# Kernel optimization log

Hardware: AMD Instinct MI355X
Metric: run time of the kernel (lower is better)

The kernel has to match this reference:

```python
import jax, jax.numpy as jnp
import numpy as np

N_GRAPHS = 8
EPS_BN = 1e-5


def _gat(x, src, dst, W, a_src, a_dst, bias, heads, out_dim):
    # PyG GATConv: linear -> per-edge leaky-relu attention -> segment softmax over dst -> scatter-sum
    N = x.shape[0]
    h = (x @ W).reshape(N, heads, out_dim)                      # [N,H,C]
    al_s = (h * a_src).sum(-1)                                  # [N,H]
    al_d = (h * a_dst).sum(-1)                                  # [N,H]
    e = jax.nn.leaky_relu(al_s[src] + al_d[dst], 0.2)           # [E,H]
    e_max = jax.ops.segment_max(e, dst, num_segments=N)         # [N,H]
    e = jnp.exp(e - e_max[dst])
    denom = jax.ops.segment_sum(e, dst, num_segments=N)         # [N,H]
    alpha = e / (denom[dst] + 1e-16)                            # [E,H]
    msg = h[src] * alpha[:, :, None]                            # [E,H,C]
    out = jax.ops.segment_sum(msg, dst, num_segments=N)         # [N,H,C]
    return out.reshape(N, heads * out_dim) + bias


def _bn(h, gamma, beta):
    # BatchNorm over nodes, training-mode (batch stats, biased var)
    m = h.mean(0)
    v = jnp.mean((h - m) ** 2, axis=0)
    return (h - m) * jax.lax.rsqrt(v + EPS_BN) * gamma + beta


def setup_inputs() -> dict:
    key = jax.random.key(0)
    ks = jax.random.split(key, 24)
    N, F, H, HD, E, B, A = 50000, 64, 4, 64, 400000, N_GRAPHS, 4
    D = H * HD  # 256
    x = jax.random.normal(ks[0], (N, F), dtype=jnp.float32)
    edge_index = jax.random.randint(ks[1], (2, E), 0, N, dtype=jnp.int32)
    batch_index = jnp.sort(jax.random.randint(ks[2], (N,), 0, B, dtype=jnp.int32))
    target_node_idx = jax.random.randint(ks[3], (B,), 0, N, dtype=jnp.int32)
    s = lambda k, shp, sc: jax.random.normal(k, shp, dtype=jnp.float32) * sc
    params = {
        "W1": s(ks[4], (F, D), 0.1), "a1_src": s(ks[5], (1, H, HD), 0.1),
        "a1_dst": s(ks[6], (1, H, HD), 0.1), "b1": jnp.zeros((D,), jnp.float32),
        "W2": s(ks[7], (D, D), 0.05), "a2_src": s(ks[8], (1, 1, D), 0.1),
        "a2_dst": s(ks[9], (1, 1, D), 0.1), "b2": jnp.zeros((D,), jnp.float32),
        "g1": jnp.ones((D,), jnp.float32), "be1": jnp.zeros((D,), jnp.float32),
        "g2": jnp.ones((D,), jnp.float32), "be2": jnp.zeros((D,), jnp.float32),
        "W_sh": s(ks[10], (D, D), 0.05), "b_sh": jnp.zeros((D,), jnp.float32),
        "W_node": s(ks[11], (2 * D, 1), 0.01), "b_node": jnp.zeros((1,), jnp.float32),
        "W_type": s(ks[12], (2 * D, A), 0.01), "b_type": jnp.zeros((A,), jnp.float32),
        "W_crit": s(ks[13], (D, 1), 0.05), "b_crit": jnp.zeros((1,), jnp.float32),
    }
    return {"x": x, "edge_index": edge_index, "batch_index": batch_index,
            "target_node_idx": target_node_idx, **params}


def reference(x, edge_index, batch_index, target_node_idx,
              W1, a1_src, a1_dst, b1, W2, a2_src, a2_dst, b2,
              g1, be1, g2, be2, W_sh, b_sh, W_node, b_node,
              W_type, b_type, W_crit, b_crit):
    N = x.shape[0]
    loop = jnp.arange(N, dtype=edge_index.dtype)  # GATConv adds self-loops by default
    src = jnp.concatenate([edge_index[0], loop])
    dst = jnp.concatenate([edge_index[1], loop])

    h = jax.nn.relu(_bn(_gat(x, src, dst, W1, a1_src, a1_dst, b1, 4, 64), g1, be1))
    x_nodes = jax.nn.relu(_bn(_gat(h, src, dst, W2, a2_src, a2_dst, b2, 1, 256), g2, be2))

    # global_mean_pool
    ones = jnp.ones((N,), x.dtype)
    cnt = jax.ops.segment_sum(ones, batch_index, num_segments=N_GRAPHS)
    sums = jax.ops.segment_sum(x_nodes, batch_index, num_segments=N_GRAPHS)
    global_feat = sums / jnp.maximum(cnt, 1.0)[:, None]          # [B,256]
    shared = jax.nn.relu(global_feat @ W_sh + b_sh)              # [B,256]

    node_ctx = jnp.concatenate([x_nodes, shared[batch_index]], axis=1)   # [N,512]
    node_scores = (node_ctx @ W_node + b_node).squeeze(-1)               # [N]

    combined = jnp.concatenate([shared, x_nodes[target_node_idx]], axis=1)  # [B,512]
    type_logits = combined @ W_type + b_type                                # [B,4]
    value = shared @ W_crit + b_crit                                        # [B,1]
    return node_scores, type_logits, value
```

## Files before the change

kernel.cpp:

```cpp
#include <hip/hip_runtime.h>

typedef unsigned short u16;
typedef __attribute__((ext_vector_type(8))) short bf16x8;
typedef __attribute__((ext_vector_type(4))) float f32x4;

#define NPART 64
#define CAP 32

__device__ __forceinline__ float bf2f(u16 u) {
    return __uint_as_float(((unsigned int)u) << 16);
}
__device__ __forceinline__ u16 f2bf(float f) {
    unsigned int u = __float_as_uint(f);
    u += 0x7fffu + ((u >> 16) & 1u);
    return (u16)(u >> 16);
}
__device__ __forceinline__ bf16x8 pack8(float4 a, float4 b) {
    bf16x8 r;
    r[0] = (short)f2bf(a.x); r[1] = (short)f2bf(a.y);
    r[2] = (short)f2bf(a.z); r[3] = (short)f2bf(a.w);
    r[4] = (short)f2bf(b.x); r[5] = (short)f2bf(b.y);
    r[6] = (short)f2bf(b.z); r[7] = (short)f2bf(b.w);
    return r;
}
__device__ __forceinline__ void fma8(float* acc, float a, int4 v) {
    unsigned vx = (unsigned)v.x, vy = (unsigned)v.y, vz = (unsigned)v.z, vw = (unsigned)v.w;
    acc[0] = fmaf(a, bf2f((u16)(vx & 0xffff)), acc[0]);
    acc[1] = fmaf(a, bf2f((u16)(vx >> 16)), acc[1]);
    acc[2] = fmaf(a, bf2f((u16)(vy & 0xffff)), acc[2]);
    acc[3] = fmaf(a, bf2f((u16)(vy >> 16)), acc[3]);
    acc[4] = fmaf(a, bf2f((u16)(vz & 0xffff)), acc[4]);
    acc[5] = fmaf(a, bf2f((u16)(vz >> 16)), acc[5]);
    acc[6] = fmaf(a, bf2f((u16)(vw & 0xffff)), acc[6]);
    acc[7] = fmaf(a, bf2f((u16)(vw >> 16)), acc[7]);
}

__global__ __launch_bounds__(256) void packW_kernel(const float* __restrict__ W1,
                                                    const float* __restrict__ W2,
                                                    u16* __restrict__ out1,
                                                    u16* __restrict__ out2,
                                                    const int* __restrict__ batch,
                                                    int N, int* __restrict__ bnds) {
    const int total1 = 16 * 2 * 512;
    const int total2 = 16 * 8 * 512;
    int idx = (int)blockIdx.x * 256 + threadIdx.x;
    if (idx >= total1 + total2) {
        int i = idx - (total1 + total2);
        if (i < N) {
            int b = batch[i];
            int bp = (i == 0) ? -1 : batch[i - 1];
            for (int g2 = bp + 1; g2 <= b; g2++) bnds[g2] = i;
            if (i == N - 1)
                for (int g2 = b + 1; g2 <= 8; g2++) bnds[g2] = N;
        }
        return;
    }
    const float* W;
    u16* out;
    int KS, id;
    if (idx < total1) { W = W1; out = out1; KS = 2; id = idx; }
    else { W = W2; out = out2; KS = 8; id = idx - total1; }
    int j = id & 7;
    int lane = (id >> 3) & 63;
    int rest = id >> 9;
    int ks = rest % KS;
    int ct = rest / KS;
    int k = ks * 32 + (lane >> 4) * 8 + j;
    int n = ct * 16 + (lane & 15);
    out[id] = f2bf(W[k * 256 + n]);
}

template <int K, int H, int MODE>
__global__ __launch_bounds__(256) void gemm_mfma(const void* __restrict__ Ain,
                                                 const u16* __restrict__ Bp,
                                                 u16* __restrict__ O,
                                                 const float* __restrict__ as_,
                                                 const float* __restrict__ ad_,
                                                 float* __restrict__ als,
                                                 float* __restrict__ ald,
                                                 const float* __restrict__ bsum,
                                                 const float* __restrict__ bsq,
                                                 const float* __restrict__ g,
                                                 const float* __restrict__ be,
                                                 int Nrows,
                                                 const int* __restrict__ ei2,
                                                 int E2,
                                                 int* __restrict__ cursor,
                                                 u16* __restrict__ csr,
                                                 int scatterBlocks) {
    constexpr int KS = K / 32;
    __shared__ u16 lds[4][32 * 256];
    __shared__ float sc_s[256], sh_s[256];
    if (MODE == 0) {
        if ((int)blockIdx.x < scatterBlocks) {
            int i = blockIdx.x * 256 + threadIdx.x;
            if (i < E2) {
                int d = ei2[E2 + i];
                int p = atomicAdd(&cursor[d], 1);
                if (p < CAP) csr[(size_t)d * CAP + p] = (u16)ei2[i];
            } else if (i < E2 + Nrows) {
                int n = i - E2;
                int p = atomicAdd(&cursor[n], 1);
                if (p < CAP) csr[(size_t)n * CAP + p] = (u16)n;
            }
            return;
        }
    }
    if (MODE == 1) {
        int t = threadIdx.x;
        float mmS = 0.f, qqS = 0.f;
        for (int k2 = 0; k2 < NPART; k2++) {
            mmS += bsum[k2 * 256 + t];
            qqS += bsq[k2 * 256 + t];
        }
        float inv = 1.f / (float)Nrows;
        float mm = mmS * inv;
        float vv = fmaxf(qqS * inv - mm * mm, 0.f);
        float sc = rsqrtf(vv + 1e-5f) * g[t];
        sc_s[t] = sc;
        sh_s[t] = be[t] - mm * sc;
        __syncthreads();
    }
    int wave = threadIdx.x >> 6, lane = threadIdx.x & 63;
    int tile = ((int)blockIdx.x - (MODE == 0 ? scatterBlocks : 0)) * 4 + wave;
    int row0 = tile * 32;
    if (row0 >= Nrows) return;
    int m = lane & 15, q = lane >> 4;
    int r0c = min(row0 + m, Nrows - 1);
    int r1c = min(row0 + 16 + m, Nrows - 1);

    bf16x8 af0[KS], af1[KS];
    if (MODE == 0) {
        const float* A = (const float*)Ain;
        const float* a0 = A + (size_t)r0c * K + q * 8;
        const float* a1 = A + (size_t)r1c * K + q * 8;
#pragma unroll
        for (int ks = 0; ks < KS; ks++) {
            af0[ks] = pack8(*(const float4*)(a0 + ks * 32), *(const float4*)(a0 + ks * 32 + 4));
            af1[ks] = pack8(*(const float4*)(a1 + ks * 32), *(const float4*)(a1 + ks * 32 + 4));
        }
    } else {
        const u16* A = (const u16*)Ain;
        const u16* a0 = A + (size_t)r0c * K + q * 8;
        const u16* a1 = A + (size_t)r1c * K + q * 8;
#pragma unroll
        for (int ks = 0; ks < KS; ks++) {
            int cb = ks * 32 + q * 8;
            float4 sc0 = *(const float4*)&sc_s[cb];
            float4 sc1 = *(const float4*)&sc_s[cb + 4];
            float4 sh0 = *(const float4*)&sh_s[cb];
            float4 sh1 = *(const float4*)&sh_s[cb + 4];
            ushort4 u0 = *(const ushort4*)(a0 + ks * 32);
            ushort4 u1 = *(const ushort4*)(a0 + ks * 32 + 4);
            float4 v0 = make_float4(fmaxf(fmaf(bf2f(u0.x), sc0.x, sh0.x), 0.f),
                                    fmaxf(fmaf(bf2f(u0.y), sc0.y, sh0.y), 0.f),
                                    fmaxf(fmaf(bf2f(u0.z), sc0.z, sh0.z), 0.f),
                                    fmaxf(fmaf(bf2f(u0.w), sc0.w, sh0.w), 0.f));
            float4 v1 = make_float4(fmaxf(fmaf(bf2f(u1.x), sc1.x, sh1.x), 0.f),
                                    fmaxf(fmaf(bf2f(u1.y), sc1.y, sh1.y), 0.f),
                                    fmaxf(fmaf(bf2f(u1.z), sc1.z, sh1.z), 0.f),
                                    fmaxf(fmaf(bf2f(u1.w), sc1.w, sh1.w), 0.f));
            af0[ks] = pack8(v0, v1);
            ushort4 w0 = *(const ushort4*)(a1 + ks * 32);
            ushort4 w1 = *(const ushort4*)(a1 + ks * 32 + 4);
            float4 x0 = make_float4(fmaxf(fmaf(bf2f(w0.x), sc0.x, sh0.x), 0.f),
                                    fmaxf(fmaf(bf2f(w0.y), sc0.y, sh0.y), 0.f),
                                    fmaxf(fmaf(bf2f(w0.z), sc0.z, sh0.z), 0.f),
                                    fmaxf(fmaf(bf2f(w0.w), sc0.w, sh0.w), 0.f));
            float4 x1 = make_float4(fmaxf(fmaf(bf2f(w1.x), sc1.x, sh1.x), 0.f),
                                    fmaxf(fmaf(bf2f(w1.y), sc1.y, sh1.y), 0.f),
                                    fmaxf(fmaf(bf2f(w1.z), sc1.z, sh1.z), 0.f),
                                    fmaxf(fmaf(bf2f(w1.w), sc1.w, sh1.w), 0.f));
            af1[ks] = pack8(x0, x1);
        }
    }

    u16* myl = lds[wave];
#pragma unroll
    for (int ct2 = 0; ct2 < 8; ct2++) {
        int ct0 = ct2 * 2;
        f32x4 a00 = {0.f, 0.f, 0.f, 0.f}, a01 = {0.f, 0.f, 0.f, 0.f};
        f32x4 a10 = {0.f, 0.f, 0.f, 0.f}, a11 = {0.f, 0.f, 0.f, 0.f};
        const u16* bp0 = Bp + ((size_t)(ct0 * KS) * 64 + lane) * 8;
        const u16* bp1 = bp0 + (size_t)KS * 512;
#pragma unroll
        for (int ks = 0; ks < KS; ks++) {
            bf16x8 b0 = *(const bf16x8*)(bp0 + (size_t)ks * 512);
            bf16x8 b1 = *(const bf16x8*)(bp1 + (size_t)ks * 512);
            a00 = __builtin_amdgcn_mfma_f32_16x16x32_bf16(af0[ks], b0, a00, 0, 0, 0);
            a01 = __builtin_amdgcn_mfma_f32_16x16x32_bf16(af0[ks], b1, a01, 0, 0, 0);
            a10 = __builtin_amdgcn_mfma_f32_16x16x32_bf16(af1[ks], b0, a10, 0, 0, 0);
            a11 = __builtin_amdgcn_mfma_f32_16x16x32_bf16(af1[ks], b1, a11, 0, 0, 0);
        }
#pragma unroll
        for (int r = 0; r < 4; r++) {
            myl[(q * 4 + r) * 256 + ct0 * 16 + m] = f2bf(a00[r]);
            myl[(q * 4 + r) * 256 + ct0 * 16 + 16 + m] = f2bf(a01[r]);
            myl[(16 + q * 4 + r) * 256 + ct0 * 16 + m] = f2bf(a10[r]);
            myl[(16 + q * 4 + r) * 256 + ct0 * 16 + 16 + m] = f2bf(a11[r]);
        }
    }
    int c8 = (lane & 31) * 8;
    float4 s0 = *(const float4*)(as_ + c8);
    float4 s1 = *(const float4*)(as_ + c8 + 4);
    float4 d0 = *(const float4*)(ad_ + c8);
    float4 d1 = *(const float4*)(ad_ + c8 + 4);
#pragma unroll
    for (int p = 0; p < 16; p++) {
        int row = p * 2 + (lane >> 5);
        if (row0 + row >= Nrows) continue;
        int4 v = *(const int4*)&myl[row * 256 + c8];
        *(int4*)&O[(size_t)(row0 + row) * 256 + c8] = v;
        float f0 = bf2f((u16)(v.x & 0xffff)), f1 = bf2f((u16)((unsigned)v.x >> 16));
        float f2 = bf2f((u16)(v.y & 0xffff)), f3 = bf2f((u16)((unsigned)v.y >> 16));
        float f4 = bf2f((u16)(v.z & 0xffff)), f5 = bf2f((u16)((unsigned)v.z >> 16));
        float f6 = bf2f((u16)(v.w & 0xffff)), f7 = bf2f((u16)((unsigned)v.w >> 16));
        float ps = f0 * s0.x + f1 * s0.y + f2 * s0.z + f3 * s0.w +
                   f4 * s1.x + f5 * s1.y + f6 * s1.z + f7 * s1.w;
        float pd = f0 * d0.x + f1 * d0.y + f2 * d0.z + f3 * d0.w +
                   f4 * d1.x + f5 * d1.y + f6 * d1.z + f7 * d1.w;
        const int W = (H == 4) ? 8 : 32;
#pragma unroll
        for (int o = 1; o < W; o <<= 1) {
            ps += __shfl_xor(ps, o);
            pd += __shfl_xor(pd, o);
        }
        if (H == 4) {
            if ((lane & 7) == 0) {
                int head = (lane & 31) >> 3;
                als[(row0 + row) * 4 + head] = ps;
                ald[(row0 + row) * 4 + head] = pd;
            }
        } else {
            if ((lane & 31) == 0) {
                als[row0 + row] = ps;
                ald[row0 + row] = pd;
            }
        }
    }
}

template <int H>
__global__ __launch_bounds__(256) void gat_fused_kernel(const int* __restrict__ cnt,
                                                        const u16* __restrict__ csr,
                                                        const float* __restrict__ als,
                                                        const float* __restrict__ ald,
                                                        const u16* __restrict__ h,
                                                        u16* __restrict__ out, int N,
                                                        float* __restrict__ sum_p,
                                                        float* __restrict__ sq_p) {
    constexpr int PRE = 12;
    __shared__ float lalpha[8][32 * H];
    __shared__ int lsrc[8][32];
    __shared__ float lbuf[8][256];
    int hw = threadIdx.x >> 5;
    int lane = threadIdx.x & 31;
    int w = (blockIdx.x * 256 + threadIdx.x) >> 5;
    bool active = (w < N);
    int wc = active ? w : (N - 1);
    int deg = active ? min(cnt[wc], CAP) : 0;
    int s0 = wc * CAP;
    int s1 = s0 + deg;
    int cend = min(deg, 32);
    int npre = min(cend, PRE);
    float adl[H], e0[H], m[H], den[H];
#pragma unroll
    for (int hh = 0; hh < H; hh++) {
        adl[hh] = active ? ald[wc * H + hh] : 0.f;
        m[hh] = -1e30f;
    }
    int i0 = s0 + lane;
    bool have = active && (i0 < s1);
    int src0 = have ? (int)csr[i0] : (active ? (int)csr[s0] : 0);
    const int4* h16 = (const int4*)h;
    int4 hreg[PRE];
#pragma unroll
    for (int j = 0; j < PRE; j++) {
        int s = __shfl(src0, j, 32);
        if (j < npre) hreg[j] = h16[(size_t)s * 32 + lane];
    }
    if (have) {
        if (H == 4) {
            float4 av = ((const float4*)als)[src0];
            float tmp[4] = {av.x, av.y, av.z, av.w};
#pragma unroll
            for (int hh = 0; hh < 4; hh++) {
                float e = tmp[hh] + adl[hh];
                e = e > 0.f ? e : 0.2f * e;
                e0[hh] = e; m[hh] = e;
            }
        } else {
            float e = als[src0] + adl[0];
            e = e > 0.f ? e : 0.2f * e;
            e0[0] = e; m[0] = e;
        }
    }
    for (int i = i0 + 32; i < s1; i += 32) {
        int s = (int)csr[i];
#pragma unroll
        for (int hh = 0; hh < H; hh++) {
            float e = als[s * H + hh] + adl[hh];
            e = e > 0.f ? e : 0.2f * e;
            m[hh] = fmaxf(m[hh], e);
        }
    }
#pragma unroll
    for (int hh = 0; hh < H; hh++)
        for (int o = 16; o; o >>= 1) m[hh] = fmaxf(m[hh], __shfl_xor(m[hh], o));
#pragma unroll
    for (int hh = 0; hh < H; hh++) den[hh] = have ? __expf(e0[hh] - m[hh]) : 0.f;
    for (int i = i0 + 32; i < s1; i += 32) {
        int s = (int)csr[i];
#pragma unroll
        for (int hh = 0; hh < H; hh++) {
            float e = als[s * H + hh] + adl[hh];
            e = e > 0.f ? e : 0.2f * e;
            den[hh] += __expf(e - m[hh]);
        }
    }
#pragma unroll
    for (int hh = 0; hh < H; hh++)
        for (int o = 16; o; o >>= 1) den[hh] += __shfl_xor(den[hh], o);
    float rden[H];
#pragma unroll
    for (int hh = 0; hh < H; hh++) rden[hh] = 1.f / (den[hh] + 1e-16f);
    if (have) {
        lsrc[hw][lane] = src0;
#pragma unroll
        for (int hh = 0; hh < H; hh++)
            lalpha[hw][lane * H + hh] = __expf(e0[hh] - m[hh]) * rden[hh];
    }
    int myh = (H == 4) ? (lane >> 3) : 0;
    const float* la = lalpha[hw];
    const int* ls = lsrc[hw];
    float acc[8];
#pragma unroll
    for (int k2 = 0; k2 < 8; k2++) acc[k2] = 0.f;
#pragma unroll
    for (int j = 0; j < PRE; j++)
        if (j < npre) fma8(acc, la[j * H + myh], hreg[j]);
    int i = npre;
    for (; i + 4 <= cend; i += 4) {
        int sa = ls[i], sb = ls[i + 1], sc = ls[i + 2], sd = ls[i + 3];
        float aa = la[i * H + myh];
        float ab = la[(i + 1) * H + myh];
        float ac = la[(i + 2) * H + myh];
        float ad = la[(i + 3) * H + myh];
        int4 ha = h16[(size_t)sa * 32 + lane];
        int4 hb = h16[(size_t)sb * 32 + lane];
        int4 hc = h16[(size_t)sc * 32 + lane];
        int4 hd = h16[(size_t)sd * 32 + lane];
        fma8(acc, aa, ha);
        fma8(acc, ab, hb);
        fma8(acc, ac, hc);
        fma8(acc, ad, hd);
    }
    for (; i < cend; i++) {
        int s = ls[i];
        float a = la[i * H + myh];
        fma8(acc, a, h16[(size_t)s * 32 + lane]);
    }
    for (int j = s0 + 32; j < s1; j++) {
        int s = (int)csr[j];
        float e = als[s * H + myh] + adl[myh];
        e = e > 0.f ? e : 0.2f * e;
        float a = __expf(e - m[myh]) * rden[myh];
        fma8(acc, a, h16[(size_t)s * 32 + lane]);
    }
    u16 ob[8];
#pragma unroll
    for (int k2 = 0; k2 < 8; k2++) ob[k2] = f2bf(acc[k2]);
    if (active) {
        int4 o;
        o.x = (int)((unsigned)ob[0] | ((unsigned)ob[1] << 16));
        o.y = (int)((unsigned)ob[2] | ((unsigned)ob[3] << 16));
        o.z = (int)((unsigned)ob[4] | ((unsigned)ob[5] << 16));
        o.w = (int)((unsigned)ob[6] | ((unsigned)ob[7] << 16));
        ((int4*)out)[(size_t)w * 32 + lane] = o;
    }
    int cbase = lane * 8;
    float vv[8];
#pragma unroll
    for (int k2 = 0; k2 < 8; k2++) vv[k2] = active ? bf2f(ob[k2]) : 0.f;
#pragma unroll
    for (int k2 = 0; k2 < 8; k2++) lbuf[hw][cbase + k2] = vv[k2];
    __syncthreads();
    int t = threadIdx.x;
    float S = 0.f;
#pragma unroll
    for (int j2 = 0; j2 < 8; j2++) S += lbuf[j2][t];
    __syncthreads();
#pragma unroll
    for (int k2 = 0; k2 < 8; k2++) lbuf[hw][cbase + k2] = vv[k2] * vv[k2];
    __syncthreads();
    float Q = 0.f;
#pragma unroll
    for (int j2 = 0; j2 < 8; j2++) Q += lbuf[j2][t];
    int part = (int)(blockIdx.x & (NPART - 1));
    atomicAdd(&sum_p[part * 256 + t], S);
    atomicAdd(&sq_p[part * 256 + t], Q);
}

__global__ __launch_bounds__(256) void bn_pool(const u16* __restrict__ agg,
                                               const float* __restrict__ sum_p,
                                               const float* __restrict__ sq_p,
                                               const float* __restrict__ g,
                                               const float* __restrict__ be,
                                               const int* __restrict__ bnds,
                                               const int* __restrict__ tgt,
                                               float* __restrict__ pools,
                                               float* __restrict__ xtgt,
                                               float* __restrict__ sc_tab,
                                               float* __restrict__ sh_tab, int N) {
    int t = threadIdx.x;
    float mmS = 0.f, qqS = 0.f;
    for (int k2 = 0; k2 < NPART; k2++) {
        mmS += sum_p[k2 * 256 + t];
        qqS += sq_p[k2 * 256 + t];
    }
    float inv = 1.f / (float)N;
    float mm = mmS * inv;
    float vv = fmaxf(qqS * inv - mm * mm, 0.f);
    float sc = rsqrtf(vv + 1e-5f) * g[t];
    float sh = be[t] - mm * sc;
    if (blockIdx.x == 0) {
        sc_tab[t] = sc;
        sh_tab[t] = sh;
    }
    int tl[8];
#pragma unroll
    for (int b = 0; b < 8; b++) tl[b] = tgt[b];
    int gid = (int)blockIdx.x >> 7;
    int sub = (int)blockIdx.x & 127;
    int gstart = bnds[gid], gend = bnds[gid + 1];
    int len = gend - gstart;
    int rows = (len + 127) >> 7;
    int r0 = gstart + sub * rows, r1 = min(r0 + rows, gend);
    if (r0 >= r1) return;
    float a0 = 0.f, a1 = 0.f, a2 = 0.f, a3 = 0.f;
    int r = r0;
    for (; r + 4 <= r1; r += 4) {
        u16 u0 = agg[(size_t)(r + 0) * 256 + t];
        u16 u1 = agg[(size_t)(r + 1) * 256 + t];
        u16 u2 = agg[(size_t)(r + 2) * 256 + t];
        u16 u3 = agg[(size_t)(r + 3) * 256 + t];
        float y0 = fmaxf(fmaf(bf2f(u0), sc, sh), 0.f);
        float y1 = fmaxf(fmaf(bf2f(u1), sc, sh), 0.f);
        float y2 = fmaxf(fmaf(bf2f(u2), sc, sh), 0.f);
        float y3 = fmaxf(fmaf(bf2f(u3), sc, sh), 0.f);
        a0 += y0; a1 += y1; a2 += y2; a3 += y3;
        float ys[4] = {y0, y1, y2, y3};
#pragma unroll
        for (int j = 0; j < 4; j++)
#pragma unroll
            for (int b2i = 0; b2i < 8; b2i++)
                if (r + j == tl[b2i]) xtgt[b2i * 256 + t] = ys[j];
    }
    for (; r < r1; r++) {
        float y = fmaxf(fmaf(bf2f(agg[(size_t)r * 256 + t]), sc, sh), 0.f);
        a0 += y;
#pragma unroll
        for (int b2i = 0; b2i < 8; b2i++)
            if (r == tl[b2i]) xtgt[b2i * 256 + t] = y;
    }
    atomicAdd(&pools[gid * 256 + t], (a0 + a1) + (a2 + a3));
}

__global__ __launch_bounds__(256) void shared_head_kernel(const float* __restrict__ pools,
                                                          const int* __restrict__ bnds,
                                                          const float* __restrict__ Wsh,
                                                          const float* __restrict__ bsh,
                                                          const float* __restrict__ Wnode,
                                                          const float* __restrict__ Wcrit,
                                                          const float* __restrict__ bcrit,
                                                          const float* __restrict__ Wtype,
                                                          const float* __restrict__ btype,
                                                          const float* __restrict__ xtgt,
                                                          float* __restrict__ gdot,
                                                          float* __restrict__ out_tail) {
    __shared__ float gf[256], red[256];
    int b = blockIdx.x, t = threadIdx.x;
    float cnt = (float)(bnds[b + 1] - bnds[b]);
    gf[t] = pools[b * 256 + t] / fmaxf(cnt, 1.f);
    __syncthreads();
    float acc = bsh[t];
    for (int k = 0; k < 256; k++) acc = fmaf(gf[k], Wsh[k * 256 + t], acc);
    float s = fmaxf(acc, 0.f);
    float xnt = xtgt[b * 256 + t];
    float pg = s * Wnode[256 + t];
    float pv = s * Wcrit[t];
    float pt0 = s * Wtype[t * 4 + 0] + xnt * Wtype[(256 + t) * 4 + 0];
    float pt1 = s * Wtype[t * 4 + 1] + xnt * Wtype[(256 + t) * 4 + 1];
    float pt2 = s * Wtype[t * 4 + 2] + xnt * Wtype[(256 + t) * 4 + 2];
    float pt3 = s * Wtype[t * 4 + 3] + xnt * Wtype[(256 + t) * 4 + 3];
    auto bred = [&](float v) -> float {
        __syncthreads();
        red[t] = v;
        __syncthreads();
        for (int o = 128; o; o >>= 1) {
            if (t < o) red[t] += red[t + o];
            __syncthreads();
        }
        return red[0];
    };
    float rg = bred(pg);
    float rv = bred(pv);
    float r0 = bred(pt0);
    float r1 = bred(pt1);
    float r2 = bred(pt2);
    float r3 = bred(pt3);
    if (t == 0) {
        gdot[b] = rg;
        out_tail[32 + b] = rv + bcrit[0];
        out_tail[b * 4 + 0] = r0 + btype[0];
        out_tail[b * 4 + 1] = r1 + btype[1];
        out_tail[b * 4 + 2] = r2 + btype[2];
        out_tail[b * 4 + 3] = r3 + btype[3];
    }
}

__global__ __launch_bounds__(256) void ndot_out(const u16* __restrict__ agg,
                                                const float* __restrict__ sc_tab,
                                                const float* __restrict__ sh_tab,
                                                const float* __restrict__ Wnode,
                                                const float* __restrict__ bnode,
                                                const int* __restrict__ batch,
                                                const float* __restrict__ gdot,
                                                float* __restrict__ out, int N) {
    int w = (blockIdx.x * 256 + threadIdx.x) >> 6;
    int lane = threadIdx.x & 63;
    if (w >= N) return;
    int c = lane * 4;
    float4 scv = *(const float4*)(sc_tab + c);
    float4 shv = *(const float4*)(sh_tab + c);
    float4 wn = *(const float4*)(Wnode + c);
    ushort4 u = *(const ushort4*)(agg + (size_t)w * 256 + c);
    float y0 = fmaxf(fmaf(bf2f(u.x), scv.x, shv.x), 0.f);
    float y1 = fmaxf(fmaf(bf2f(u.y), scv.y, shv.y), 0.f);
    float y2 = fmaxf(fmaf(bf2f(u.z), scv.z, shv.z), 0.f);
    float y3 = fmaxf(fmaf(bf2f(u.w), scv.w, shv.w), 0.f);
    float p = y0 * wn.x + y1 * wn.y + y2 * wn.z + y3 * wn.w;
#pragma unroll
    for (int o = 32; o; o >>= 1) p += __shfl_xor(p, o);
    if (lane == 0) out[w] = p + gdot[batch[w]] + bnode[0];
}

extern "C" void kernel_launch(void* const* d_in, const int* in_sizes, int n_in,
                              void* d_out, int out_size, void* d_ws, size_t ws_size,
                              hipStream_t stream) {
    const float* x = (const float*)d_in[0];
    const int* ei = (const int*)d_in[1];
    const int* batch = (const int*)d_in[2];
    const int* tgt = (const int*)d_in[3];
    const float* W1 = (const float*)d_in[4];
    const float* a1s = (const float*)d_in[5];
    const float* a1d = (const float*)d_in[6];
    const float* W2 = (const float*)d_in[8];
    const float* a2s = (const float*)d_in[9];
    const float* a2d = (const float*)d_in[10];
    const float* g1 = (const float*)d_in[12];
    const float* be1 = (const float*)d_in[13];
    const float* g2 = (const float*)d_in[14];
    const float* be2 = (const float*)d_in[15];
    const float* Wsh = (const float*)d_in[16];
    const float* bsh = (const float*)d_in[17];
    const float* Wnode = (const float*)d_in[18];
    const float* bnode = (const float*)d_in[19];
    const float* Wtype = (const float*)d_in[20];
    const float* btype = (const float*)d_in[21];
    const float* Wcrit = (const float*)d_in[22];
    const float* bcrit = (const float*)d_in[23];

    const int N = in_sizes[2];
    const int E = in_sizes[1] / 2;
    const int Et = E + N;

    char* w = (char*)d_ws;
    size_t off = 0;
    auto carve = [&](size_t bytes) -> char* {
        char* p = w + off;
        off = (off + bytes + 255) & ~(size_t)255;
        return p;
    };
    u16* agg_bf = (u16*)carve((size_t)N * 256 * 2);
    u16* h_bf = (u16*)carve((size_t)N * 256 * 2);
    u16* W1p = (u16*)carve(16 * 2 * 512 * 2);
    u16* W2p = (u16*)carve(16 * 8 * 512 * 2);
    float* al1s = (float*)carve((size_t)N * 4 * 4);
    float* al1d = (float*)carve((size_t)N * 4 * 4);
    float* al2s = (float*)carve((size_t)N * 4);
    float* al2d = (float*)carve((size_t)N * 4);
    float* xtgt = (float*)carve(8 * 256 * 4);
    float* sc_tab = (float*)carve(1024);
    float* sh_tab = (float*)carve(1024);
    u16* csr = (u16*)carve((size_t)N * CAP * 2);
    int* bnds = (int*)carve(64);
    float* gdot = (float*)carve(64);
    char* zero0 = w + off;
    int* cursor = (int*)carve((size_t)N * 4);
    float* bn1s = (float*)carve(NPART * 256 * 4);
    float* bn1q = (float*)carve(NPART * 256 * 4);
    float* bn2s = (float*)carve(NPART * 256 * 4);
    float* bn2q = (float*)carve(NPART * 256 * 4);
    float* pools = (float*)carve(8 * 256 * 4);
    size_t zbytes = (size_t)((w + off) - zero0);
    hipMemsetAsync(zero0, 0, zbytes, stream);

    int halfGrid = (N + 7) / 8;
    int mfmaGrid = (((N + 31) / 32) + 3) / 4;
    int packBlocks = (16 * 10 * 512 + N + 255) / 256;
    int scatterBlocks = (Et + 255) / 256;

    packW_kernel<<<packBlocks, 256, 0, stream>>>(W1, W2, W1p, W2p, batch, N, bnds);

    gemm_mfma<64, 4, 0><<<scatterBlocks + mfmaGrid, 256, 0, stream>>>(
        x, W1p, h_bf, a1s, a1d, al1s, al1d, bn1s, bn1q, g1, be1, N,
        ei, E, cursor, csr, scatterBlocks);
    gat_fused_kernel<4><<<halfGrid, 256, 0, stream>>>(cursor, csr, al1s, al1d, h_bf, agg_bf, N,
                                                      bn1s, bn1q);

    gemm_mfma<256, 1, 1><<<mfmaGrid, 256, 0, stream>>>(agg_bf, W2p, h_bf, a2s, a2d, al2s, al2d,
                                                       bn1s, bn1q, g1, be1, N,
                                                       nullptr, 0, nullptr, nullptr, 0);
    gat_fused_kernel<1><<<halfGrid, 256, 0, stream>>>(cursor, csr, al2s, al2d, h_bf, agg_bf, N,
                                                      bn2s, bn2q);
    bn_pool<<<1024, 256, 0, stream>>>(agg_bf, bn2s, bn2q, g2, be2, bnds, tgt,
                                      pools, xtgt, sc_tab, sh_tab, N);

    shared_head_kernel<<<8, 256, 0, stream>>>(pools, bnds, Wsh, bsh, Wnode, Wcrit, bcrit,
                                              Wtype, btype, xtgt, gdot, (float*)d_out + N);
    ndot_out<<<(N + 3) / 4, 256, 0, stream>>>(agg_bf, sc_tab, sh_tab, Wnode, bnode,
                                              batch, gdot, (float*)d_out, N);
}
```

Baseline: 294.7 us.

## Fuse BN-pool, shared head and node-score kernels into one cooperative kernel

Replaces the three tail kernels (bn_pool, shared_head_kernel, ndot_out) with a single cooperative launch of 1024 blocks that uses grid-wide syncs between the pooling, head and per-node score phases. BN scale and shift stay in shared memory instead of a global table, and the per-node dot product becomes a grid-stride loop over waves. This removes two kernel launches and the gaps between them. In exchange it pays two grid barriers, leaves most blocks idle during the head phase, and requires all 1024 blocks to be resident at once.

```diff
diff --git a/kernel.cpp b/kernel.cpp
--- a/kernel.cpp
+++ b/kernel.cpp
@@ -1,4 +1,7 @@
 #include <hip/hip_runtime.h>
+#include <hip/hip_cooperative_groups.h>
+
+namespace cg = cooperative_groups;
 
 typedef unsigned short u16;
 typedef __attribute__((ext_vector_type(8))) short bf16x8;
@@ -401,17 +404,30 @@
     atomicAdd(&sq_p[part * 256 + t], Q);
 }
 
-__global__ __launch_bounds__(256) void bn_pool(const u16* __restrict__ agg,
-                                               const float* __restrict__ sum_p,
-                                               const float* __restrict__ sq_p,
-                                               const float* __restrict__ g,
-                                               const float* __restrict__ be,
-                                               const int* __restrict__ bnds,
-                                               const int* __restrict__ tgt,
-                                               float* __restrict__ pools,
-                                               float* __restrict__ xtgt,
-                                               float* __restrict__ sc_tab,
-                                               float* __restrict__ sh_tab, int N) {
+__global__ __launch_bounds__(256) void tail_coop(const u16* __restrict__ agg,
+                                                 const float* __restrict__ sum_p,
+                                                 const float* __restrict__ sq_p,
+                                                 const float* __restrict__ g,
+                                                 const float* __restrict__ be,
+                                                 const int* __restrict__ bnds,
+                                                 const int* __restrict__ tgt,
+                                                 float* __restrict__ pools,
+                                                 float* __restrict__ xtgt,
+                                                 const float* __restrict__ Wsh,
+                                                 const float* __restrict__ bsh,
+                                                 const float* __restrict__ Wnode,
+                                                 const float* __restrict__ bnode,
+                                                 const float* __restrict__ Wcrit,
+                                                 const float* __restrict__ bcrit,
+                                                 const float* __restrict__ Wtype,
+                                                 const float* __restrict__ btype,
+                                                 const int* __restrict__ batch,
+                                                 float* __restrict__ gdot,
+                                                 float* __restrict__ out_tail,
+                                                 float* __restrict__ out, int N) {
+    cg::grid_group grid = cg::this_grid();
+    __shared__ float scs[256], shs[256];
+    __shared__ float gf[256], red[256];
     int t = threadIdx.x;
     float mmS = 0.f, qqS = 0.f;
     for (int k2 = 0; k2 < NPART; k2++) {
@@ -423,126 +439,111 @@
     float vv = fmaxf(qqS * inv - mm * mm, 0.f);
     float sc = rsqrtf(vv + 1e-5f) * g[t];
     float sh = be[t] - mm * sc;
-    if (blockIdx.x == 0) {
-        sc_tab[t] = sc;
-        sh_tab[t] = sh;
-    }
-    int tl[8];
-#pragma unroll
-    for (int b = 0; b < 8; b++) tl[b] = tgt[b];
-    int gid = (int)blockIdx.x >> 7;
-    int sub = (int)blockIdx.x & 127;
-    int gstart = bnds[gid], gend = bnds[gid + 1];
-    int len = gend - gstart;
-    int rows = (len + 127) >> 7;
-    int r0 = gstart + sub * rows, r1 = min(r0 + rows, gend);
-    if (r0 >= r1) return;
-    float a0 = 0.f, a1 = 0.f, a2 = 0.f, a3 = 0.f;
-    int r = r0;
-    for (; r + 4 <= r1; r += 4) {
-        u16 u0 = agg[(size_t)(r + 0) * 256 + t];
-        u16 u1 = agg[(size_t)(r + 1) * 256 + t];
-        u16 u2 = agg[(size_t)(r + 2) * 256 + t];
-        u16 u3 = agg[(size_t)(r + 3) * 256 + t];
-        float y0 = fmaxf(fmaf(bf2f(u0), sc, sh), 0.f);
-        float y1 = fmaxf(fmaf(bf2f(u1), sc, sh), 0.f);
-        float y2 = fmaxf(fmaf(bf2f(u2), sc, sh), 0.f);
-        float y3 = fmaxf(fmaf(bf2f(u3), sc, sh), 0.f);
-        a0 += y0; a1 += y1; a2 += y2; a3 += y3;
-        float ys[4] = {y0, y1, y2, y3};
-#pragma unroll
-        for (int j = 0; j < 4; j++)
-#pragma unroll
-            for (int b2i = 0; b2i < 8; b2i++)
-                if (r + j == tl[b2i]) xtgt[b2i * 256 + t] = ys[j];
-    }
-    for (; r < r1; r++) {
-        float y = fmaxf(fmaf(bf2f(agg[(size_t)r * 256 + t]), sc, sh), 0.f);
-        a0 += y;
-#pragma unroll
-        for (int b2i = 0; b2i < 8; b2i++)
-            if (r == tl[b2i]) xtgt[b2i * 256 + t] = y;
-    }
-    atomicAdd(&pools[gid * 256 + t], (a0 + a1) + (a2 + a3));
-}
-
-__global__ __launch_bounds__(256) void shared_head_kernel(const float* __restrict__ pools,
-                                                          const int* __restrict__ bnds,
-                                                          const float* __restrict__ Wsh,
-                                                          const float* __restrict__ bsh,
-                                                          const float* __restrict__ Wnode,
-                                                          const float* __restrict__ Wcrit,
-                                                          const float* __restrict__ bcrit,
-                                                          const float* __restrict__ Wtype,
-                                                          const float* __restrict__ btype,
-                                                          const float* __restrict__ xtgt,
-                                                          float* __restrict__ gdot,
-                                                          float* __restrict__ out_tail) {
-    __shared__ float gf[256], red[256];
-    int b = blockIdx.x, t = threadIdx.x;
-    float cnt = (float)(bnds[b + 1] - bnds[b]);
-    gf[t] = pools[b * 256 + t] / fmaxf(cnt, 1.f);
-    __syncthreads();
-    float acc = bsh[t];
-    for (int k = 0; k < 256; k++) acc = fmaf(gf[k], Wsh[k * 256 + t], acc);
-    float s = fmaxf(acc, 0.f);
-    float xnt = xtgt[b * 256 + t];
-    float pg = s * Wnode[256 + t];
-    float pv = s * Wcrit[t];
-    float pt0 = s * Wtype[t * 4 + 0] + xnt * Wtype[(256 + t) * 4 + 0];
-    float pt1 = s * Wtype[t * 4 + 1] + xnt * Wtype[(256 + t) * 4 + 1];
-    float pt2 = s * Wtype[t * 4 + 2] + xnt * Wtype[(256 + t) * 4 + 2];
-    float pt3 = s * Wtype[t * 4 + 3] + xnt * Wtype[(256 + t) * 4 + 3];
-    auto bred = [&](float v) -> float {
+    scs[t] = sc;
+    shs[t] = sh;
+    {
+        int tl[8];
+#pragma unroll
+        for (int b = 0; b < 8; b++) tl[b] = tgt[b];
+        int gid = (int)blockIdx.x >> 7;
+        int sub = (int)blockIdx.x & 127;
+        int gstart = bnds[gid], gend = bnds[gid + 1];
+        int len = gend - gstart;
+        int rows = (len + 127) >> 7;
+        int r0 = gstart + sub * rows, r1 = min(r0 + rows, gend);
+        if (r0 < r1) {
+            float a0 = 0.f, a1 = 0.f, a2 = 0.f, a3 = 0.f;
+            int r = r0;
+            for (; r + 4 <= r1; r += 4) {
+                u16 u0 = agg[(size_t)(r + 0) * 256 + t];
+                u16 u1 = agg[(size_t)(r + 1) * 256 + t];
+                u16 u2 = agg[(size_t)(r + 2) * 256 + t];
+                u16 u3 = agg[(size_t)(r + 3) * 256 + t];
+                float y0 = fmaxf(fmaf(bf2f(u0), sc, sh), 0.f);
+                float y1 = fmaxf(fmaf(bf2f(u1), sc, sh), 0.f);
+                float y2 = fmaxf(fmaf(bf2f(u2), sc, sh), 0.f);
+                float y3 = fmaxf(fmaf(bf2f(u3), sc, sh), 0.f);
+                a0 += y0; a1 += y1; a2 += y2; a3 += y3;
+                float ys[4] = {y0, y1, y2, y3};
+#pragma unroll
+                for (int j = 0; j < 4; j++)
+#pragma unroll
+                    for (int b2i = 0; b2i < 8; b2i++)
+                        if (r + j == tl[b2i]) xtgt[b2i * 256 + t] = ys[j];
+            }
+            for (; r < r1; r++) {
+                float y = fmaxf(fmaf(bf2f(agg[(size_t)r * 256 + t]), sc, sh), 0.f);
+                a0 += y;
+#pragma unroll
+                for (int b2i = 0; b2i < 8; b2i++)
+                    if (r == tl[b2i]) xtgt[b2i * 256 + t] = y;
+            }
+            atomicAdd(&pools[gid * 256 + t], (a0 + a1) + (a2 + a3));
+        }
+    }
+    grid.sync();
+    if ((int)blockIdx.x < 8) {
+        int b = blockIdx.x;
+        float cnt = (float)(bnds[b + 1] - bnds[b]);
+        gf[t] = pools[b * 256 + t] / fmaxf(cnt, 1.f);
         __syncthreads();
-        red[t] = v;
-        __syncthreads();
-        for (int o = 128; o; o >>= 1) {
-            if (t < o) red[t] += red[t + o];
+        float acc = bsh[t];
+        for (int k = 0; k < 256; k++) acc = fmaf(gf[k], Wsh[k * 256 + t], acc);
+        float s = fmaxf(acc, 0.f);
+        float xnt = xtgt[b * 256 + t];
+        float pg = s * Wnode[256 + t];
+        float pv = s * Wcrit[t];
+        float pt0 = s * Wtype[t * 4 + 0] + xnt * Wtype[(256 + t) * 4 + 0];
+        float pt1 = s * Wtype[t * 4 + 1] + xnt * Wtype[(256 + t) * 4 + 1];
+        float pt2 = s * Wtype[t * 4 + 2] + xnt * Wtype[(256 + t) * 4 + 2];
+        float pt3 = s * Wtype[t * 4 + 3] + xnt * Wtype[(256 + t) * 4 + 3];
+        auto bred = [&](float v) -> float {
             __syncthreads();
-        }
-        return red[0];
-    };
-    float rg = bred(pg);
-    float rv = bred(pv);
-    float r0 = bred(pt0);
-    float r1 = bred(pt1);
-    float r2 = bred(pt2);
-    float r3 = bred(pt3);
-    if (t == 0) {
-        gdot[b] = rg;
-        out_tail[32 + b] = rv + bcrit[0];
-        out_tail[b * 4 + 0] = r0 + btype[0];
-        out_tail[b * 4 + 1] = r1 + btype[1];
-        out_tail[b * 4 + 2] = r2 + btype[2];
-        out_tail[b * 4 + 3] = r3 + btype[3];
-    }
-}
-
-__global__ __launch_bounds__(256) void ndot_out(const u16* __restrict__ agg,
-                                                const float* __restrict__ sc_tab,
-                                                const float* __restrict__ sh_tab,
-                                                const float* __restrict__ Wnode,
-                                                const float* __restrict__ bnode,
-                                                const int* __restrict__ batch,
-                                                const float* __restrict__ gdot,
-                                                float* __restrict__ out, int N) {
-    int w = (blockIdx.x * 256 + threadIdx.x) >> 6;
-    int lane = threadIdx.x & 63;
-    if (w >= N) return;
-    int c = lane * 4;
-    float4 scv = *(const float4*)(sc_tab + c);
-    float4 shv = *(const float4*)(sh_tab + c);
-    float4 wn = *(const float4*)(Wnode + c);
-    ushort4 u = *(const ushort4*)(agg + (size_t)w * 256 + c);
-    float y0 = fmaxf(fmaf(bf2f(u.x), scv.x, shv.x), 0.f);
-    float y1 = fmaxf(fmaf(bf2f(u.y), scv.y, shv.y), 0.f);
-    float y2 = fmaxf(fmaf(bf2f(u.z), scv.z, shv.z), 0.f);
-    float y3 = fmaxf(fmaf(bf2f(u.w), scv.w, shv.w), 0.f);
-    float p = y0 * wn.x + y1 * wn.y + y2 * wn.z + y3 * wn.w;
-#pragma unroll
-    for (int o = 32; o; o >>= 1) p += __shfl_xor(p, o);
-    if (lane == 0) out[w] = p + gdot[batch[w]] + bnode[0];
+            red[t] = v;
+            __syncthreads();
+            for (int o = 128; o; o >>= 1) {
+                if (t < o) red[t] += red[t + o];
+                __syncthreads();
+            }
+            return red[0];
+        };
+        float rg = bred(pg);
+        float rv = bred(pv);
+        float r0 = bred(pt0);
+        float r1 = bred(pt1);
+        float r2 = bred(pt2);
+        float r3 = bred(pt3);
+        if (t == 0) {
+            gdot[b] = rg;
+            out_tail[32 + b] = rv + bcrit[0];
+            out_tail[b * 4 + 0] = r0 + btype[0];
+            out_tail[b * 4 + 1] = r1 + btype[1];
+            out_tail[b * 4 + 2] = r2 + btype[2];
+            out_tail[b * 4 + 3] = r3 + btype[3];
+        }
+    }
+    grid.sync();
+    {
+        int lane = t & 63;
+        int c = lane * 4;
+        float4 scv = *(const float4*)&scs[c];
+        float4 shv = *(const float4*)&shs[c];
+        float4 wn = *(const float4*)(Wnode + c);
+        float bn0 = bnode[0];
+        int gwave = (int)((blockIdx.x * 256 + t) >> 6);
+        int nw = (int)gridDim.x * 4;
+        for (int w = gwave; w < N; w += nw) {
+            ushort4 u = *(const ushort4*)(agg + (size_t)w * 256 + c);
+            float y0 = fmaxf(fmaf(bf2f(u.x), scv.x, shv.x), 0.f);
+            float y1 = fmaxf(fmaf(bf2f(u.y), scv.y, shv.y), 0.f);
+            float y2 = fmaxf(fmaf(bf2f(u.z), scv.z, shv.z), 0.f);
+            float y3 = fmaxf(fmaf(bf2f(u.w), scv.w, shv.w), 0.f);
+            float p = y0 * wn.x + y1 * wn.y + y2 * wn.z + y3 * wn.w;
+#pragma unroll
+            for (int o = 32; o; o >>= 1) p += __shfl_xor(p, o);
+            if (lane == 0) out[w] = p + gdot[batch[w]] + bn0;
+        }
+    }
 }
 
 extern "C" void kernel_launch(void* const* d_in, const int* in_sizes, int n_in,
@@ -591,8 +592,6 @@
     float* al2s = (float*)carve((size_t)N * 4);
     float* al2d = (float*)carve((size_t)N * 4);
     float* xtgt = (float*)carve(8 * 256 * 4);
-    float* sc_tab = (float*)carve(1024);
-    float* sh_tab = (float*)carve(1024);
     u16* csr = (u16*)carve((size_t)N * CAP * 2);
     int* bnds = (int*)carve(64);
     float* gdot = (float*)carve(64);
@@ -624,11 +623,19 @@
                                                        nullptr, 0, nullptr, nullptr, 0);
     gat_fused_kernel<1><<<halfGrid, 256, 0, stream>>>(cursor, csr, al2s, al2d, h_bf, agg_bf, N,
                                                       bn2s, bn2q);
-    bn_pool<<<1024, 256, 0, stream>>>(agg_bf, bn2s, bn2q, g2, be2, bnds, tgt,
-                                      pools, xtgt, sc_tab, sh_tab, N);
-
-    shared_head_kernel<<<8, 256, 0, stream>>>(pools, bnds, Wsh, bsh, Wnode, Wcrit, bcrit,
-                                              Wtype, btype, xtgt, gdot, (float*)d_out + N);
-    ndot_out<<<(N + 3) / 4, 256, 0, stream>>>(agg_bf, sc_tab, sh_tab, Wnode, bnode,
-                                              batch, gdot, (float*)d_out, N);
-}
+
+    {
+        float* out_scores = (float*)d_out;
+        float* out_tail = (float*)d_out + N;
+        int Nv = N;
+        void* args[] = {(void*)&agg_bf, (void*)&bn2s, (void*)&bn2q,
+                        (void*)&g2, (void*)&be2, (void*)&bnds, (void*)&tgt,
+                        (void*)&pools, (void*)&xtgt,
+                        (void*)&Wsh, (void*)&bsh, (void*)&Wnode, (void*)&bnode,
+                        (void*)&Wcrit, (void*)&bcrit, (void*)&Wtype, (void*)&btype,
+                        (void*)&batch, (void*)&gdot, (void*)&out_tail,
+                        (void*)&out_scores, (void*)&Nv};
+        hipLaunchCooperativeKernel((const void*)tail_coop, dim3(1024), dim3(256),
+                                   args, 0, stream);
+    }
+}
```

New measurement: 528.4 us. 79.3% more time.
